# Performance work log

Hardware: AMD Instinct MI355X
Metric: run time of the kernel (lower is better)

The kernel has to match this reference:

```python
import jax, jax.numpy as jnp
import numpy as np

IN_FEATURES = 4096
OUT_FEATURES = 11008
GROUP_SIZE = 128


def setup_inputs() -> dict:
    key = jax.random.key(0)
    k_x, k_w, k_s, k_z, k_b = jax.random.split(key, 5)
    x = jax.random.normal(k_x, (8, IN_FEATURES), dtype=jnp.float32)
    # packed INT4 weights: two 4-bit values per byte, stored in int32 (0..255)
    weight_q = jax.random.randint(k_w, (OUT_FEATURES, IN_FEATURES // 2), 0, 256, dtype=jnp.int32)
    num_groups = IN_FEATURES // GROUP_SIZE  # 32
    scales = jax.random.uniform(k_s, (OUT_FEATURES, num_groups), dtype=jnp.float32) * 0.01 + 1e-4
    zeros = jax.random.normal(k_z, (OUT_FEATURES, num_groups), dtype=jnp.float32) * 0.05
    bias = jax.random.normal(k_b, (OUT_FEATURES,), dtype=jnp.float32) * 0.02
    return {"x": x, "weight_q": weight_q, "scales": scales, "zeros": zeros, "bias": bias}


def _dequantize(weight_q, scales, zeros):
    # unpack INT4: low nibble first, then high nibble (matches torch stack order)
    low = weight_q & 15
    high = (weight_q >> 4) & 15
    q = jnp.stack([low, high], axis=-1).reshape(OUT_FEATURES, -1)  # [out, in]
    q = q.astype(scales.dtype)
    num_groups = scales.shape[1]
    q = q[:, : num_groups * GROUP_SIZE].reshape(OUT_FEATURES, num_groups, GROUP_SIZE)
    w = q * scales[:, :, None] + zeros[:, :, None]
    return w.reshape(OUT_FEATURES, -1)[:, :IN_FEATURES]


def reference(x, weight_q, scales, zeros, bias):
    w = _dequantize(weight_q, scales, zeros)            # [out, in]
    return x.astype(w.dtype) @ w.T + bias               # [B, out]
```

## Files before the change

kernel.cpp:

```cpp
#include <hip/hip_runtime.h>

typedef _Float16 f16;
typedef __attribute__((ext_vector_type(2))) _Float16 f16x2;
typedef __attribute__((ext_vector_type(4))) _Float16 f16x4;
typedef __attribute__((ext_vector_type(8))) _Float16 f16x8;
typedef __attribute__((ext_vector_type(4))) float f32x4;
typedef __attribute__((ext_vector_type(4))) unsigned u32x4;

constexpr int IN_F  = 4096;
constexpr int OUT_F = 11008;
constexpr int NGRP  = 32;

__global__ void xprep_kernel(const float* __restrict__ x, f16* __restrict__ xh) {
    int i = (blockIdx.x * blockDim.x + threadIdx.x) * 4;
    float4 v = *(const float4*)(x + i);
    f16x4 r = {(f16)v.x, (f16)v.y, (f16)v.z, (f16)v.w};
    *(f16x4*)(xh + i) = r;
}

__device__ __forceinline__ unsigned dq2(unsigned q, f16x2 sp, f16x2 zp) {
    unsigned t = (((q << 12) | q) & 0x000F000Fu) | 0x64006400u;
    f16x2 u = __builtin_bit_cast(f16x2, t);
    u = u - (f16x2){(_Float16)1024.0f, (_Float16)1024.0f};
    u = u * sp + zp;
    return __builtin_bit_cast(unsigned, u);
}

__device__ __forceinline__ f16x2 bcast(float v) {
    _Float16 h = (_Float16)v;
    return (f16x2){h, h};
}

template<bool PRE>
__global__ __launch_bounds__(256, 4)
void qlin_kernel(const int* __restrict__ wq,
                 const float* __restrict__ scales,
                 const float* __restrict__ zeros,
                 const float* __restrict__ bias,
                 const float* __restrict__ xf,
                 const f16* __restrict__ xh,
                 float* __restrict__ out)
{
    __shared__ unsigned char wlds[2][16][1024];
    __shared__ f32x4 red[4][64];

    const int tid  = threadIdx.x;
    const int wv   = tid >> 6;
    const int lane = tid & 63;
    const int col  = lane & 15;
    const int kg   = lane >> 4;
    const int o0   = blockIdx.x * 16;
    const int orow = o0 + col;
    const bool mvalid = (col < 8);

    f16x2 sp[8], zp[8];
    #pragma unroll
    for (int s = 0; s < 8; ++s) {
        sp[s] = bcast(scales[(size_t)orow * NGRP + s * 4 + wv]);
        zp[s] = bcast(zeros [(size_t)orow * NGRP + s * 4 + wv]);
    }

    const char* wtile = (const char*)wq + (size_t)o0 * 8192;

    auto stage = [&](int sl, int bufi) {
        #pragma unroll
        for (int c = 0; c < 4; ++c) {
            const int r = 4 * wv + c;
            const char* src = wtile + (size_t)r * 8192 + sl * 1024
                              + ((lane * 16) ^ ((r & 7) << 4));
            __builtin_amdgcn_global_load_lds(
                (const __attribute__((address_space(1))) void*)src,
                (__attribute__((address_space(3))) void*)&wlds[bufi][r][0],
                16, 0, 0);
        }
    };

    stage(0, 0);

    const f16*   xcol  = xh + (size_t)col * IN_F;
    const float* xfcol = xf + (size_t)col * IN_F;
    const unsigned swz = (unsigned)((col & 7) << 4);

    f32x4 acc = {0.f, 0.f, 0.f, 0.f};

    __syncthreads();

    #pragma unroll
    for (int s = 0; s < 8; ++s) {
        const int cur = s & 1;
        if (s < 7) stage(s + 1, cur ^ 1);

        f16x8 af[4];
        #pragma unroll
        for (int t = 0; t < 4; ++t) {
            const int k = s * 512 + wv * 128 + t * 32 + kg * 8;
            if (mvalid) {
                if constexpr (PRE) {
                    af[t] = *(const f16x8*)(xcol + k);
                } else {
                    float4 a0 = *(const float4*)(xfcol + k);
                    float4 a1 = *(const float4*)(xfcol + k + 4);
                    af[t] = (f16x8){(f16)a0.x,(f16)a0.y,(f16)a0.z,(f16)a0.w,
                                    (f16)a1.x,(f16)a1.y,(f16)a1.z,(f16)a1.w};
                }
            } else {
                af[t] = (f16x8){0,0,0,0,0,0,0,0};
            }
        }

        const f16x2 s2 = sp[s], z2 = zp[s];
        #pragma unroll
        for (int t = 0; t < 4; ++t) {
            const unsigned off = ((unsigned)(wv * 256 + t * 64 + kg * 16)) ^ swz;
            const int4 q = *(const int4*)&wlds[cur][col][off];
            u32x4 bw = {dq2((unsigned)q.x, s2, z2),
                        dq2((unsigned)q.y, s2, z2),
                        dq2((unsigned)q.z, s2, z2),
                        dq2((unsigned)q.w, s2, z2)};
            f16x8 bfr = __builtin_bit_cast(f16x8, bw);
            acc = __builtin_amdgcn_mfma_f32_16x16x32_f16(af[t], bfr, acc, 0, 0, 0);
        }

        __syncthreads();
    }

    red[wv][lane] = acc;
    __syncthreads();

    if (tid < 64) {
        f32x4 ssum = red[0][tid];
        #pragma unroll
        for (int w = 1; w < 4; ++w) ssum += red[w][tid];
        const int n = tid & 15;
        const float bb = bias[o0 + n];
        const int mbase = (tid >> 4) * 4;
        if (mbase < 8) {
            #pragma unroll
            for (int i = 0; i < 4; ++i)
                out[(size_t)(mbase + i) * OUT_F + o0 + n] = ssum[i] + bb;
        }
    }
}

extern "C" void kernel_launch(void* const* d_in, const int* in_sizes, int n_in,
                              void* d_out, int out_size, void* d_ws, size_t ws_size,
                              hipStream_t stream) {
    const float* x  = (const float*)d_in[0];
    const int*   wq = (const int*)d_in[1];
    const float* sc = (const float*)d_in[2];
    const float* zr = (const float*)d_in[3];
    const float* bs = (const float*)d_in[4];
    float* out = (float*)d_out;

    if (ws_size >= (size_t)(8 * IN_F * sizeof(f16))) {
        f16* xh = (f16*)d_ws;
        xprep_kernel<<<(8 * IN_F) / (256 * 4), 256, 0, stream>>>(x, xh);
        qlin_kernel<true><<<OUT_F / 16, 256, 0, stream>>>(wq, sc, zr, bs, x, xh, out);
    } else {
        qlin_kernel<false><<<OUT_F / 16, 256, 0, stream>>>(wq, sc, zr, bs, x, (const f16*)d_ws, out);
    }
}
```

Measured before the change: 30.42 us.

## Drop x pre-conversion kernel and prefetch two weight stages ahead with vmcnt waits

```diff
diff --git a/kernel.cpp b/kernel.cpp
--- a/kernel.cpp
+++ b/kernel.cpp
@@ -2,7 +2,6 @@
 
 typedef _Float16 f16;
 typedef __attribute__((ext_vector_type(2))) _Float16 f16x2;
-typedef __attribute__((ext_vector_type(4))) _Float16 f16x4;
 typedef __attribute__((ext_vector_type(8))) _Float16 f16x8;
 typedef __attribute__((ext_vector_type(4))) float f32x4;
 typedef __attribute__((ext_vector_type(4))) unsigned u32x4;
@@ -10,13 +9,6 @@
 constexpr int IN_F  = 4096;
 constexpr int OUT_F = 11008;
 constexpr int NGRP  = 32;
-
-__global__ void xprep_kernel(const float* __restrict__ x, f16* __restrict__ xh) {
-    int i = (blockIdx.x * blockDim.x + threadIdx.x) * 4;
-    float4 v = *(const float4*)(x + i);
-    f16x4 r = {(f16)v.x, (f16)v.y, (f16)v.z, (f16)v.w};
-    *(f16x4*)(xh + i) = r;
-}
 
 __device__ __forceinline__ unsigned dq2(unsigned q, f16x2 sp, f16x2 zp) {
     unsigned t = (((q << 12) | q) & 0x000F000Fu) | 0x64006400u;
@@ -31,14 +23,12 @@
     return (f16x2){h, h};
 }
 
-template<bool PRE>
 __global__ __launch_bounds__(256, 4)
 void qlin_kernel(const int* __restrict__ wq,
                  const float* __restrict__ scales,
                  const float* __restrict__ zeros,
                  const float* __restrict__ bias,
                  const float* __restrict__ xf,
-                 const f16* __restrict__ xh,
                  float* __restrict__ out)
 {
     __shared__ unsigned char wlds[2][16][1024];
@@ -76,52 +66,44 @@
     };
 
     stage(0, 0);
+    stage(1, 1);
 
-    const f16*   xcol  = xh + (size_t)col * IN_F;
     const float* xfcol = xf + (size_t)col * IN_F;
     const unsigned swz = (unsigned)((col & 7) << 4);
 
     f32x4 acc = {0.f, 0.f, 0.f, 0.f};
 
-    __syncthreads();
-
     #pragma unroll
     for (int s = 0; s < 8; ++s) {
-        const int cur = s & 1;
-        if (s < 7) stage(s + 1, cur ^ 1);
-
-        f16x8 af[4];
-        #pragma unroll
-        for (int t = 0; t < 4; ++t) {
-            const int k = s * 512 + wv * 128 + t * 32 + kg * 8;
-            if (mvalid) {
-                if constexpr (PRE) {
-                    af[t] = *(const f16x8*)(xcol + k);
-                } else {
-                    float4 a0 = *(const float4*)(xfcol + k);
-                    float4 a1 = *(const float4*)(xfcol + k + 4);
-                    af[t] = (f16x8){(f16)a0.x,(f16)a0.y,(f16)a0.z,(f16)a0.w,
-                                    (f16)a1.x,(f16)a1.y,(f16)a1.z,(f16)a1.w};
-                }
-            } else {
-                af[t] = (f16x8){0,0,0,0,0,0,0,0};
-            }
-        }
+        if (s < 7) asm volatile("s_waitcnt vmcnt(4)" ::: "memory");
+        else       asm volatile("s_waitcnt vmcnt(0)" ::: "memory");
+        __builtin_amdgcn_s_barrier();
+        asm volatile("" ::: "memory");
 
         const f16x2 s2 = sp[s], z2 = zp[s];
         #pragma unroll
         for (int t = 0; t < 4; ++t) {
+            const int k = s * 512 + wv * 128 + t * 32 + kg * 8;
+            f16x8 af = (f16x8){0,0,0,0,0,0,0,0};
+            if (mvalid) {
+                float4 a0 = *(const float4*)(xfcol + k);
+                float4 a1 = *(const float4*)(xfcol + k + 4);
+                af = (f16x8){(f16)a0.x,(f16)a0.y,(f16)a0.z,(f16)a0.w,
+                             (f16)a1.x,(f16)a1.y,(f16)a1.z,(f16)a1.w};
+            }
             const unsigned off = ((unsigned)(wv * 256 + t * 64 + kg * 16)) ^ swz;
-            const int4 q = *(const int4*)&wlds[cur][col][off];
+            const int4 q = *(const int4*)&wlds[s & 1][col][off];
             u32x4 bw = {dq2((unsigned)q.x, s2, z2),
                         dq2((unsigned)q.y, s2, z2),
                         dq2((unsigned)q.z, s2, z2),
                         dq2((unsigned)q.w, s2, z2)};
             f16x8 bfr = __builtin_bit_cast(f16x8, bw);
-            acc = __builtin_amdgcn_mfma_f32_16x16x32_f16(af[t], bfr, acc, 0, 0, 0);
+            acc = __builtin_amdgcn_mfma_f32_16x16x32_f16(af, bfr, acc, 0, 0, 0);
         }
 
-        __syncthreads();
+        asm volatile("" ::: "memory");
+        __builtin_amdgcn_s_barrier();
+        if (s < 6) stage(s + 2, s & 1);
     }
 
     red[wv][lane] = acc;
@@ -151,12 +133,7 @@
     const float* zr = (const float*)d_in[3];
     const float* bs = (const float*)d_in[4];
     float* out = (float*)d_out;
+    (void)d_ws; (void)ws_size; (void)in_sizes; (void)n_in;
 
-    if (ws_size >= (size_t)(8 * IN_F * sizeof(f16))) {
-        f16* xh = (f16*)d_ws;
-        xprep_kernel<<<(8 * IN_F) / (256 * 4), 256, 0, stream>>>(x, xh);
-        qlin_kernel<true><<<OUT_F / 16, 256, 0, stream>>>(wq, sc, zr, bs, x, xh, out);
-    } else {
-        qlin_kernel<false><<<OUT_F / 16, 256, 0, stream>>>(wq, sc, zr, bs, x, (const f16*)d_ws, out);
-    }
+    qlin_kernel<<<OUT_F / 16, 256, 0, stream>>>(wq, sc, zr, bs, x, out);
 }
```

After: 31.70 us. +4.2%, slower.

## Split K across eight blocks per output tile and combine with atomics

Applied to the files above, without the earlier changes.

```diff
diff --git a/kernel.cpp b/kernel.cpp
--- a/kernel.cpp
+++ b/kernel.cpp
@@ -10,13 +10,7 @@
 constexpr int IN_F  = 4096;
 constexpr int OUT_F = 11008;
 constexpr int NGRP  = 32;
-
-__global__ void xprep_kernel(const float* __restrict__ x, f16* __restrict__ xh) {
-    int i = (blockIdx.x * blockDim.x + threadIdx.x) * 4;
-    float4 v = *(const float4*)(x + i);
-    f16x4 r = {(f16)v.x, (f16)v.y, (f16)v.z, (f16)v.w};
-    *(f16x4*)(xh + i) = r;
-}
+constexpr int NTILE = OUT_F / 16;
 
 __device__ __forceinline__ unsigned dq2(unsigned q, f16x2 sp, f16x2 zp) {
     unsigned t = (((q << 12) | q) & 0x000F000Fu) | 0x64006400u;
@@ -31,14 +25,103 @@
     return (f16x2){h, h};
 }
 
-template<bool PRE>
+__global__ void xprep_kernel(const float* __restrict__ x, f16* __restrict__ xh) {
+    int i = (blockIdx.x * blockDim.x + threadIdx.x) * 4;
+    float4 v = *(const float4*)(x + i);
+    f16x4 r = {(f16)v.x, (f16)v.y, (f16)v.z, (f16)v.w};
+    *(f16x4*)(xh + i) = r;
+}
+
+__global__ __launch_bounds__(256, 6)
+void qlin_atomic(const int* __restrict__ wq,
+                 const float* __restrict__ scales,
+                 const float* __restrict__ zeros,
+                 const float* __restrict__ bias,
+                 const f16* __restrict__ xh,
+                 float* __restrict__ out)
+{
+    __shared__ unsigned char wlds[16384];
+
+    const int tid  = threadIdx.x;
+    const int wv   = tid >> 6;
+    const int lane = tid & 63;
+    const int col  = lane & 15;
+    const int kg   = lane >> 4;
+    const int bid  = blockIdx.x;
+    const int ot   = bid >> 3;
+    const int ks   = bid & 7;
+    const int o0   = ot * 16;
+    const int orow = o0 + col;
+    const int k0   = ks * 512 + wv * 128;
+    const int g    = k0 >> 7;
+    const bool mvalid = (col < 8);
+
+    const char* wb = (const char*)wq;
+    #pragma unroll
+    for (int c = 0; c < 4; ++c) {
+        const int r = c * 4 + (lane >> 4);
+        const char* src = wb + (size_t)(o0 + r) * 8192 + (size_t)k0 * 2
+                          + (((lane & 15) * 16) ^ ((r & 7) << 4));
+        __builtin_amdgcn_global_load_lds(
+            (const __attribute__((address_space(1))) void*)src,
+            (__attribute__((address_space(3))) void*)&wlds[wv * 4096 + c * 1024],
+            16, 0, 0);
+    }
+
+    f16x8 af[4];
+    if (mvalid) {
+        const f16* xp = xh + (size_t)col * IN_F + k0 + kg * 8;
+        #pragma unroll
+        for (int t = 0; t < 4; ++t) af[t] = *(const f16x8*)(xp + t * 32);
+    } else {
+        #pragma unroll
+        for (int t = 0; t < 4; ++t) af[t] = (f16x8){0,0,0,0,0,0,0,0};
+    }
+
+    const f16x2 s2 = bcast(scales[(size_t)orow * NGRP + g]);
+    const f16x2 z2 = bcast(zeros [(size_t)orow * NGRP + g]);
+
+    asm volatile("s_waitcnt vmcnt(0)" ::: "memory");
+    __builtin_amdgcn_sched_barrier(0);
+
+    const unsigned swz  = (unsigned)((col & 7) << 4);
+    const unsigned base = (unsigned)(wv * 4096 + col * 256);
+    f32x4 acc = {0.f, 0.f, 0.f, 0.f};
+    #pragma unroll
+    for (int t = 0; t < 4; ++t) {
+        const unsigned off = base + (((unsigned)(t * 64 + kg * 16)) ^ swz);
+        const int4 q = *(const int4*)&wlds[off];
+        u32x4 bw = {dq2((unsigned)q.x, s2, z2),
+                    dq2((unsigned)q.y, s2, z2),
+                    dq2((unsigned)q.z, s2, z2),
+                    dq2((unsigned)q.w, s2, z2)};
+        f16x8 bfr = __builtin_bit_cast(f16x8, bw);
+        acc = __builtin_amdgcn_mfma_f32_16x16x32_f16(af[t], bfr, acc, 0, 0, 0);
+    }
+
+    *(f32x4*)&wlds[wv * 4096 + lane * 16] = acc;
+    __syncthreads();
+
+    if (tid < 32) {
+        f32x4 ssum = *(const f32x4*)&wlds[tid * 16];
+        #pragma unroll
+        for (int w = 1; w < 4; ++w)
+            ssum += *(const f32x4*)&wlds[w * 4096 + tid * 16];
+        const int n = tid & 15;
+        const int mbase = (tid >> 4) * 4;
+        const float bb = (ks == 0) ? bias[o0 + n] : 0.f;
+        #pragma unroll
+        for (int i = 0; i < 4; ++i)
+            atomicAdd(&out[(size_t)(mbase + i) * OUT_F + o0 + n], ssum[i] + bb);
+    }
+}
+
 __global__ __launch_bounds__(256, 4)
 void qlin_kernel(const int* __restrict__ wq,
                  const float* __restrict__ scales,
                  const float* __restrict__ zeros,
                  const float* __restrict__ bias,
                  const float* __restrict__ xf,
-                 const f16* __restrict__ xh,
                  float* __restrict__ out)
 {
     __shared__ unsigned char wlds[2][16][1024];
@@ -61,7 +144,6 @@
     }
 
     const char* wtile = (const char*)wq + (size_t)o0 * 8192;
-
     auto stage = [&](int sl, int bufi) {
         #pragma unroll
         for (int c = 0; c < 4; ++c) {
@@ -76,52 +158,42 @@
     };
 
     stage(0, 0);
-
-    const f16*   xcol  = xh + (size_t)col * IN_F;
+    stage(1, 1);
+
     const float* xfcol = xf + (size_t)col * IN_F;
     const unsigned swz = (unsigned)((col & 7) << 4);
-
     f32x4 acc = {0.f, 0.f, 0.f, 0.f};
 
-    __syncthreads();
-
     #pragma unroll
     for (int s = 0; s < 8; ++s) {
-        const int cur = s & 1;
-        if (s < 7) stage(s + 1, cur ^ 1);
-
-        f16x8 af[4];
+        asm volatile("s_waitcnt vmcnt(0)" ::: "memory");
+        __builtin_amdgcn_s_barrier();
+        asm volatile("" ::: "memory");
+
+        const f16x2 s2 = sp[s], z2 = zp[s];
         #pragma unroll
         for (int t = 0; t < 4; ++t) {
             const int k = s * 512 + wv * 128 + t * 32 + kg * 8;
+            f16x8 af = (f16x8){0,0,0,0,0,0,0,0};
             if (mvalid) {
-                if constexpr (PRE) {
-                    af[t] = *(const f16x8*)(xcol + k);
-                } else {
-                    float4 a0 = *(const float4*)(xfcol + k);
-                    float4 a1 = *(const float4*)(xfcol + k + 4);
-                    af[t] = (f16x8){(f16)a0.x,(f16)a0.y,(f16)a0.z,(f16)a0.w,
-                                    (f16)a1.x,(f16)a1.y,(f16)a1.z,(f16)a1.w};
-                }
-            } else {
-                af[t] = (f16x8){0,0,0,0,0,0,0,0};
+                float4 a0 = *(const float4*)(xfcol + k);
+                float4 a1 = *(const float4*)(xfcol + k + 4);
+                af = (f16x8){(f16)a0.x,(f16)a0.y,(f16)a0.z,(f16)a0.w,
+                             (f16)a1.x,(f16)a1.y,(f16)a1.z,(f16)a1.w};
             }
-        }
-
-        const f16x2 s2 = sp[s], z2 = zp[s];
-        #pragma unroll
-        for (int t = 0; t < 4; ++t) {
             const unsigned off = ((unsigned)(wv * 256 + t * 64 + kg * 16)) ^ swz;
-            const int4 q = *(const int4*)&wlds[cur][col][off];
+            const int4 q = *(const int4*)&wlds[s & 1][col][off];
             u32x4 bw = {dq2((unsigned)q.x, s2, z2),
                         dq2((unsigned)q.y, s2, z2),
                         dq2((unsigned)q.z, s2, z2),
                         dq2((unsigned)q.w, s2, z2)};
             f16x8 bfr = __builtin_bit_cast(f16x8, bw);
-            acc = __builtin_amdgcn_mfma_f32_16x16x32_f16(af[t], bfr, acc, 0, 0, 0);
+            acc = __builtin_amdgcn_mfma_f32_16x16x32_f16(af, bfr, acc, 0, 0, 0);
         }
 
-        __syncthreads();
+        asm volatile("" ::: "memory");
+        __builtin_amdgcn_s_barrier();
+        if (s < 6) stage(s + 2, s & 1);
     }
 
     red[wv][lane] = acc;
@@ -151,12 +223,14 @@
     const float* zr = (const float*)d_in[3];
     const float* bs = (const float*)d_in[4];
     float* out = (float*)d_out;
+    (void)in_sizes; (void)n_in;
 
     if (ws_size >= (size_t)(8 * IN_F * sizeof(f16))) {
         f16* xh = (f16*)d_ws;
+        hipMemsetAsync(out, 0, (size_t)out_size * sizeof(float), stream);
         xprep_kernel<<<(8 * IN_F) / (256 * 4), 256, 0, stream>>>(x, xh);
-        qlin_kernel<true><<<OUT_F / 16, 256, 0, stream>>>(wq, sc, zr, bs, x, xh, out);
+        qlin_atomic<<<NTILE * 8, 256, 0, stream>>>(wq, sc, zr, bs, xh, out);
     } else {
-        qlin_kernel<false><<<OUT_F / 16, 256, 0, stream>>>(wq, sc, zr, bs, x, (const f16*)d_ws, out);
-    }
-}
+        qlin_kernel<<<NTILE, 256, 0, stream>>>(wq, sc, zr, bs, x, out);
+    }
+}
```

Measured after the change: 30.01 us. No clear change (-1.3%).
